# Performance work log

Measured on AMD Instinct MI355X. Metric: run time of the kernel, lower is better.

The kernel has to match this reference:

```python
import jax, jax.numpy as jnp
import numpy as np

D = 1024
H = 16
HD = D // H
FF = 4096
B = 4
S = 1024
EPS = 1e-5


def layer_norm(x, g, b):
    mu = jnp.mean(x, axis=-1, keepdims=True)
    var = jnp.mean(jnp.square(x - mu), axis=-1, keepdims=True)
    return (x - mu) * jax.lax.rsqrt(var + EPS) * g + b


def setup_inputs() -> dict:
    key = jax.random.key(0)
    ks = jax.random.split(key, 16)
    s = 0.02
    return {
        "src": jax.random.normal(ks[0], (B, S, D), jnp.float32),
        "attn_bias": jax.random.normal(ks[1], (H, S, S), jnp.float32),
        "Wqkv": jax.random.normal(ks[2], (3 * D, D), jnp.float32) * s,
        "bqkv": jnp.zeros((3 * D,), jnp.float32),
        "Wo": jax.random.normal(ks[3], (D, D), jnp.float32) * s,
        "bo": jnp.zeros((D,), jnp.float32),
        "g1": jnp.ones((D,), jnp.float32),
        "b1n": jnp.zeros((D,), jnp.float32),
        "g2": jnp.ones((D,), jnp.float32),
        "b2n": jnp.zeros((D,), jnp.float32),
        "W1": jax.random.normal(ks[4], (FF, D), jnp.float32) * s,
        "b1": jnp.zeros((FF,), jnp.float32),
        "W2": jax.random.normal(ks[5], (D, FF), jnp.float32) * s,
        "b2": jnp.zeros((D,), jnp.float32),
    }


def reference(src, attn_bias, Wqkv, bqkv, Wo, bo, g1, b1n, g2, b2n, W1, b1, W2, b2):
    bsz, seq, _ = src.shape
    qkv = src @ Wqkv.T + bqkv                      # [B,S,3D]
    q, k, v = jnp.split(qkv, 3, axis=-1)
    q = q.reshape(bsz, seq, H, HD)
    k = k.reshape(bsz, seq, H, HD)
    v = v.reshape(bsz, seq, H, HD)
    scores = jnp.einsum('bthd,bshd->bhts', q, k) / np.sqrt(HD).astype(np.float32)
    scores = scores + attn_bias[None]              # 3D bias broadcast over batch
    w = jax.nn.softmax(scores, axis=-1)
    ctx = jnp.einsum('bhts,bshd->bthd', w, v).reshape(bsz, seq, D)
    attn_out = ctx @ Wo.T + bo
    x = layer_norm(src + attn_out, g1, b1n)
    ff = (jax.nn.gelu(x @ W1.T + b1, approximate=False)) @ W2.T + b2
    return layer_norm(x + ff, g2, b2n)
```

## Files before the change

kernel.cpp:

```cpp
#include <hip/hip_runtime.h>
#include <cstdint>

typedef unsigned short u16;
typedef __bf16 bf16x8 __attribute__((ext_vector_type(8)));
typedef float f32x4 __attribute__((ext_vector_type(4)));
typedef unsigned short u16x8 __attribute__((ext_vector_type(8)));
typedef unsigned short u16x4 __attribute__((ext_vector_type(4)));

__device__ __forceinline__ u16 f2b(float f) {
  union { float f; unsigned u; } x; x.f = f;
  unsigned r = (x.u + 0x7FFFu + ((x.u >> 16) & 1u)) >> 16;
  return (u16)r;
}
__device__ __forceinline__ float b2f(u16 v) {
  union { unsigned u; float f; } x; x.u = (unsigned)v << 16; return x.f;
}

__device__ __forceinline__ void gload_lds16(const void* g, void* l) {
  __builtin_amdgcn_global_load_lds(
      (__attribute__((address_space(1))) void*)(uintptr_t)g,
      (__attribute__((address_space(3))) void*)(uintptr_t)l, 16, 0, 0);
}

struct CastArgs {
  const float* in[5];
  u16* out[5];
  int cum[6];
};
__global__ void cast_multi(CastArgs a) {
  const int i = blockIdx.x * 256 + threadIdx.x;
  int r = 0;
#pragma unroll
  for (int k = 1; k < 5; ++k) r += (i >= a.cum[k]);
  const int local = i - a.cum[r];
  const float4 v = *(const float4*)(a.in[r] + (size_t)local * 4);
  u16x4 o = {f2b(v.x), f2b(v.y), f2b(v.z), f2b(v.w)};
  *(u16x4*)(a.out[r] + (size_t)local * 4) = o;
}

template<bool GELU_ACT>
__global__ void gemm_nt(const u16* __restrict__ A, const u16* __restrict__ Bw,
                        const float* __restrict__ bias, u16* __restrict__ Cb,
                        int M, int N, int K) {
  __shared__ u16 As[2][128 * 32];
  __shared__ u16 Bs[2][128 * 32];
  const int tid = threadIdx.x;
  const int lane = tid & 63, wid = tid >> 6;
  const int bm = blockIdx.y * 128, bn = blockIdx.x * 128;
  const int wm = wid >> 1, wn = wid & 1;
  const int r = lane & 15, g = lane >> 4;
  const int s4 = (r >> 1) & 3;

  auto stage = [&](int buf, int k0) {
#pragma unroll
    for (int i = 0; i < 2; ++i) {
      const int c = tid + i * 256;
      const int row = c >> 2, ch = c & 3;
      const int gs = ch ^ ((row >> 1) & 3);
      gload_lds16(A + (size_t)(bm + row) * K + k0 + gs * 8, &As[buf][c * 8]);
      gload_lds16(Bw + (size_t)(bn + row) * K + k0 + gs * 8, &Bs[buf][c * 8]);
    }
  };

  f32x4 acc[4][4] = {};
  stage(0, 0);
  __syncthreads();
  const int nk = K >> 5;
  int cur = 0;
  for (int kt = 0; kt < nk; ++kt) {
    if (kt + 1 < nk) stage(cur ^ 1, (kt + 1) * 32);
    bf16x8 af[4], bfr[4];
#pragma unroll
    for (int m = 0; m < 4; ++m)
      af[m] = *(const bf16x8*)&As[cur][(wm * 64 + m * 16 + r) * 32 + (g ^ s4) * 8];
#pragma unroll
    for (int n = 0; n < 4; ++n)
      bfr[n] = *(const bf16x8*)&Bs[cur][(wn * 64 + n * 16 + r) * 32 + (g ^ s4) * 8];
#pragma unroll
    for (int m = 0; m < 4; ++m)
#pragma unroll
      for (int n = 0; n < 4; ++n)
        acc[m][n] = __builtin_amdgcn_mfma_f32_16x16x32_bf16(af[m], bfr[n], acc[m][n], 0, 0, 0);
    __syncthreads();
    cur ^= 1;
  }
#pragma unroll
  for (int m = 0; m < 4; ++m) {
    const int row0 = bm + wm * 64 + m * 16 + g * 4;
#pragma unroll
    for (int n = 0; n < 4; ++n) {
      const int col = bn + wn * 64 + n * 16 + r;
      const float bv = bias[col];
#pragma unroll
      for (int j = 0; j < 4; ++j) {
        float v = acc[m][n][j] + bv;
        if (GELU_ACT) v = 0.5f * v * (1.f + erff(v * 0.70710678118654752f));
        Cb[(size_t)(row0 + j) * N + col] = f2b(v);
      }
    }
  }
}

__global__ void gemm_nt_splitk(const u16* __restrict__ A, const u16* __restrict__ Bw,
                               float* __restrict__ parts, int M, int N, int K, int Kc) {
  __shared__ u16 As[2][128 * 32];
  __shared__ u16 Bs[2][128 * 32];
  const int tid = threadIdx.x;
  const int lane = tid & 63, wid = tid >> 6;
  const int bm = blockIdx.y * 128, bn = blockIdx.x * 128;
  const int kbase = blockIdx.z * Kc;
  const int wm = wid >> 1, wn = wid & 1;
  const int r = lane & 15, g = lane >> 4;
  const int s4 = (r >> 1) & 3;

  auto stage = [&](int buf, int k0) {
#pragma unroll
    for (int i = 0; i < 2; ++i) {
      const int c = tid + i * 256;
      const int row = c >> 2, ch = c & 3;
      const int gs = ch ^ ((row >> 1) & 3);
      gload_lds16(A + (size_t)(bm + row) * K + k0 + gs * 8, &As[buf][c * 8]);
      gload_lds16(Bw + (size_t)(bn + row) * K + k0 + gs * 8, &Bs[buf][c * 8]);
    }
  };

  f32x4 acc[4][4] = {};
  stage(0, kbase);
  __syncthreads();
  const int nk = Kc >> 5;
  int cur = 0;
  for (int kt = 0; kt < nk; ++kt) {
    if (kt + 1 < nk) stage(cur ^ 1, kbase + (kt + 1) * 32);
    bf16x8 af[4], bfr[4];
#pragma unroll
    for (int m = 0; m < 4; ++m)
      af[m] = *(const bf16x8*)&As[cur][(wm * 64 + m * 16 + r) * 32 + (g ^ s4) * 8];
#pragma unroll
    for (int n = 0; n < 4; ++n)
      bfr[n] = *(const bf16x8*)&Bs[cur][(wn * 64 + n * 16 + r) * 32 + (g ^ s4) * 8];
#pragma unroll
    for (int m = 0; m < 4; ++m)
#pragma unroll
      for (int n = 0; n < 4; ++n)
        acc[m][n] = __builtin_amdgcn_mfma_f32_16x16x32_bf16(af[m], bfr[n], acc[m][n], 0, 0, 0);
    __syncthreads();
    cur ^= 1;
  }
  float* Cp = parts + (size_t)blockIdx.z * M * N;
#pragma unroll
  for (int m = 0; m < 4; ++m) {
    const int row0 = bm + wm * 64 + m * 16 + g * 4;
#pragma unroll
    for (int n = 0; n < 4; ++n) {
      const int col = bn + wn * 64 + n * 16 + r;
#pragma unroll
      for (int j = 0; j < 4; ++j)
        Cp[(size_t)(row0 + j) * N + col] = acc[m][n][j];
    }
  }
}

__global__ void vtrans_kernel(const u16* __restrict__ qkv, u16* __restrict__ Vt) {
  const int bh = blockIdx.y, b = bh >> 4, h = bh & 15;
  const int s0 = blockIdx.x * 128;
  const int tid = threadIdx.x;
  __shared__ u16 t[128][66];
#pragma unroll
  for (int i = 0; i < 32; ++i) {
    const int e = tid + i * 256;
    const int s = e >> 6, d = e & 63;
    t[s][d] = qkv[(size_t)(b * 1024 + s0 + s) * 3072 + 2048 + h * 64 + d];
  }
  __syncthreads();
#pragma unroll
  for (int i = 0; i < 4; ++i) {
    const int c = tid + i * 256;
    const int d = c >> 4, scol = (c & 15) * 8;
    u16x8 v;
#pragma unroll
    for (int j = 0; j < 8; ++j) v[j] = t[scol + j][d];
    *(u16x8*)(Vt + ((size_t)bh * 64 + d) * 1024 + s0 + scol) = v;
  }
}

__global__ __launch_bounds__(256) void attn_kernel(
    const u16* __restrict__ qkv, const u16* __restrict__ Vt,
    const float* __restrict__ bias, u16* __restrict__ ctx) {
  const int yy = blockIdx.y;
  const int h = yy >> 2, b = yy & 3;
  const int q0 = blockIdx.x * 32;
  const int tid = threadIdx.x;
  const int lane = tid & 63, wid = tid >> 6;
  const int r = lane & 15, g = lane >> 4;
  const int bh = b * 16 + h;

  __shared__ __align__(16) u16 PB[2][16 * 1024];

  const size_t qb0 = (size_t)(b * 1024 + q0 + r) * 3072 + h * 64;
  const size_t qb1 = (size_t)(b * 1024 + q0 + 16 + r) * 3072 + h * 64;
  const bf16x8 aq00 = *(const bf16x8*)(qkv + qb0 + g * 8);
  const bf16x8 aq01 = *(const bf16x8*)(qkv + qb0 + 32 + g * 8);
  const bf16x8 aq10 = *(const bf16x8*)(qkv + qb1 + g * 8);
  const bf16x8 aq11 = *(const bf16x8*)(qkv + qb1 + 32 + g * 8);

  const int n0 = wid * 256;

#pragma unroll 4
  for (int nt = 0; nt < 16; ++nt) {
    const int key = n0 + nt * 16 + r;
    const size_t kbase = (size_t)(b * 1024 + key) * 3072 + 1024 + h * 64;
    const bf16x8 bk0 = *(const bf16x8*)(qkv + kbase + g * 8);
    const bf16x8 bk1 = *(const bf16x8*)(qkv + kbase + 32 + g * 8);
    f32x4 a0 = {0.f, 0.f, 0.f, 0.f}, a1 = {0.f, 0.f, 0.f, 0.f};
    a0 = __builtin_amdgcn_mfma_f32_16x16x32_bf16(bk0, aq00, a0, 0, 0, 0);
    a1 = __builtin_amdgcn_mfma_f32_16x16x32_bf16(bk0, aq10, a1, 0, 0, 0);
    a0 = __builtin_amdgcn_mfma_f32_16x16x32_bf16(bk1, aq01, a0, 0, 0, 0);
    a1 = __builtin_amdgcn_mfma_f32_16x16x32_bf16(bk1, aq11, a1, 0, 0, 0);
    const int col = n0 + nt * 16 + g * 4;
    const int idx = r * 1024 + (col ^ ((r & 15) << 3));
    u16x4 o0 = {f2b(a0[0] * 0.125f), f2b(a0[1] * 0.125f),
                f2b(a0[2] * 0.125f), f2b(a0[3] * 0.125f)};
    u16x4 o1 = {f2b(a1[0] * 0.125f), f2b(a1[1] * 0.125f),
                f2b(a1[2] * 0.125f), f2b(a1[3] * 0.125f)};
    *(u16x4*)&PB[0][idx] = o0;
    *(u16x4*)&PB[1][idx] = o1;
  }
  __syncthreads();

#pragma unroll
  for (int tr = 0; tr < 8; ++tr) {
    const int t = tr & 1, rr = tr >> 1;
    const int row = wid * 4 + rr;
    const int swz = (row & 15) << 3;
    u16* prow = &PB[t][row * 1024];
    const float* brow = bias + ((size_t)h * 1024 + q0 + t * 16 + row) * 1024;
    const int c0 = lane * 16;
    float bb[16];
    *(float4*)&bb[0]  = *(const float4*)(brow + c0);
    *(float4*)&bb[4]  = *(const float4*)(brow + c0 + 4);
    *(float4*)&bb[8]  = *(const float4*)(brow + c0 + 8);
    *(float4*)&bb[12] = *(const float4*)(brow + c0 + 12);
    const u16x8 v0 = *(const u16x8*)&prow[c0 ^ swz];
    const u16x8 v1 = *(const u16x8*)&prow[(c0 + 8) ^ swz];
    float f[16];
#pragma unroll
    for (int k = 0; k < 8; ++k) {
      f[k]     = b2f(v0[k]) + bb[k];
      f[8 + k] = b2f(v1[k]) + bb[8 + k];
    }
    float m = f[0];
#pragma unroll
    for (int k = 1; k < 16; ++k) m = fmaxf(m, f[k]);
    m = fmaxf(m, __shfl_xor(m, 1));  m = fmaxf(m, __shfl_xor(m, 2));
    m = fmaxf(m, __shfl_xor(m, 4));  m = fmaxf(m, __shfl_xor(m, 8));
    m = fmaxf(m, __shfl_xor(m, 16)); m = fmaxf(m, __shfl_xor(m, 32));
    float s = 0.f;
#pragma unroll
    for (int k = 0; k < 16; ++k) { f[k] = __expf(f[k] - m); s += f[k]; }
    s += __shfl_xor(s, 1);  s += __shfl_xor(s, 2);
    s += __shfl_xor(s, 4);  s += __shfl_xor(s, 8);
    s += __shfl_xor(s, 16); s += __shfl_xor(s, 32);
    const float inv = 1.f / s;
    u16x8 o0, o1;
#pragma unroll
    for (int k = 0; k < 8; ++k) {
      o0[k] = f2b(f[k] * inv);
      o1[k] = f2b(f[8 + k] * inv);
    }
    *(u16x8*)&prow[c0 ^ swz] = o0;
    *(u16x8*)&prow[(c0 + 8) ^ swz] = o1;
  }
  __syncthreads();

  f32x4 oa = {0.f, 0.f, 0.f, 0.f}, ob = {0.f, 0.f, 0.f, 0.f};
  const u16* vrow = Vt + ((size_t)bh * 64 + wid * 16 + r) * 1024;
#pragma unroll 4
  for (int ks = 0; ks < 32; ++ks) {
    const int off = (ks * 32 + g * 8) ^ ((r & 15) << 3);
    const bf16x8 vb = *(const bf16x8*)(vrow + ks * 32 + g * 8);
    const bf16x8 pa0 = *(const bf16x8*)&PB[0][r * 1024 + off];
    const bf16x8 pa1 = *(const bf16x8*)&PB[1][r * 1024 + off];
    oa = __builtin_amdgcn_mfma_f32_16x16x32_bf16(pa0, vb, oa, 0, 0, 0);
    ob = __builtin_amdgcn_mfma_f32_16x16x32_bf16(pa1, vb, ob, 0, 0, 0);
  }
#pragma unroll
  for (int j = 0; j < 4; ++j) {
    ctx[(size_t)(b * 1024 + q0 + g * 4 + j) * 1024 + h * 64 + wid * 16 + r] = f2b(oa[j]);
    ctx[(size_t)(b * 1024 + q0 + 16 + g * 4 + j) * 1024 + h * 64 + wid * 16 + r] = f2b(ob[j]);
  }
}

template<int NP>
__global__ void ln_sum_kernel(const float* __restrict__ parts,
                              const float* __restrict__ resid,
                              const float* __restrict__ cbias,
                              const float* __restrict__ gw, const float* __restrict__ bw,
                              float* __restrict__ outf, u16* __restrict__ outb) {
  const int row = blockIdx.x, tid = threadIdx.x;
  const size_t off = (size_t)row * 1024 + tid * 4;
  float4 v = *(const float4*)(resid + off);
  const float4 cb = *(const float4*)(cbias + tid * 4);
  v.x += cb.x; v.y += cb.y; v.z += cb.z; v.w += cb.w;
#pragma unroll
  for (int p = 0; p < NP; ++p) {
    const float4 a = *(const float4*)(parts + (size_t)p * 4096 * 1024 + off);
    v.x += a.x; v.y += a.y; v.z += a.z; v.w += a.w;
  }
  float s = v.x + v.y + v.z + v.w;
  float q = v.x * v.x + v.y * v.y + v.z * v.z + v.w * v.w;
#pragma unroll
  for (int m = 32; m >= 1; m >>= 1) { s += __shfl_xor(s, m); q += __shfl_xor(q, m); }
  __shared__ float rs[4], rq[4];
  if ((tid & 63) == 0) { rs[tid >> 6] = s; rq[tid >> 6] = q; }
  __syncthreads();
  s = rs[0] + rs[1] + rs[2] + rs[3];
  q = rq[0] + rq[1] + rq[2] + rq[3];
  const float mu = s * (1.f / 1024.f);
  const float inv = rsqrtf(q * (1.f / 1024.f) - mu * mu + 1e-5f);
  const float4 g4 = *(const float4*)(gw + tid * 4);
  const float4 b4 = *(const float4*)(bw + tid * 4);
  float4 o;
  o.x = (v.x - mu) * inv * g4.x + b4.x;
  o.y = (v.y - mu) * inv * g4.y + b4.y;
  o.z = (v.z - mu) * inv * g4.z + b4.z;
  o.w = (v.w - mu) * inv * g4.w + b4.w;
  if (outf) *(float4*)(outf + off) = o;
  if (outb) {
    u16x4 ob = {f2b(o.x), f2b(o.y), f2b(o.z), f2b(o.w)};
    *(u16x4*)(outb + off) = ob;
  }
}

extern "C" void kernel_launch(void* const* d_in, const int* in_sizes, int n_in,
                              void* d_out, int out_size, void* d_ws, size_t ws_size,
                              hipStream_t stream) {
  (void)in_sizes; (void)n_in; (void)out_size; (void)ws_size;
  const float* src   = (const float*)d_in[0];
  const float* abias = (const float*)d_in[1];
  const float* Wqkv  = (const float*)d_in[2];
  const float* bqkv  = (const float*)d_in[3];
  const float* Wo    = (const float*)d_in[4];
  const float* bo    = (const float*)d_in[5];
  const float* g1    = (const float*)d_in[6];
  const float* b1n   = (const float*)d_in[7];
  const float* g2    = (const float*)d_in[8];
  const float* b2n   = (const float*)d_in[9];
  const float* W1    = (const float*)d_in[10];
  const float* b1    = (const float*)d_in[11];
  const float* W2    = (const float*)d_in[12];
  const float* b2    = (const float*)d_in[13];
  float* out = (float*)d_out;

  char* ws = (char*)d_ws;
  const size_t MB = 1024 * 1024;
  u16* srcb  = (u16*)(ws + 0 * MB);
  u16* ctxb  = (u16*)(ws + 0 * MB);
  u16* xb    = (u16*)(ws + 0 * MB);
  u16* Wqkvb = (u16*)(ws + 8 * MB);
  u16* Wob   = (u16*)(ws + 14 * MB);
  float* xf  = (float*)(ws + 8 * MB);
  u16* W2b   = (u16*)(ws + 24 * MB);
  u16* qkvb  = (u16*)(ws + 32 * MB);
  u16* Vt    = (u16*)(ws + 56 * MB);
  u16* hb    = (u16*)(ws + 32 * MB);
  float* parts = (float*)(ws + 64 * MB);
  u16* W1b   = (u16*)(ws + 96 * MB);

  CastArgs ca;
  ca.in[0] = src;  ca.out[0] = srcb;
  ca.in[1] = Wqkv; ca.out[1] = Wqkvb;
  ca.in[2] = Wo;   ca.out[2] = Wob;
  ca.in[3] = W1;   ca.out[3] = W1b;
  ca.in[4] = W2;   ca.out[4] = W2b;
  ca.cum[0] = 0;
  ca.cum[1] = 1048576;
  ca.cum[2] = 1048576 + 786432;
  ca.cum[3] = 1048576 + 786432 + 262144;
  ca.cum[4] = 1048576 + 786432 + 262144 + 1048576;
  ca.cum[5] = 4194304;
  cast_multi<<<4194304 / 256, 256, 0, stream>>>(ca);

  gemm_nt<false><<<dim3(3072 / 128, 4096 / 128), 256, 0, stream>>>(
      srcb, Wqkvb, bqkv, qkvb, 4096, 3072, 1024);
  vtrans_kernel<<<dim3(8, 64), 256, 0, stream>>>(qkvb, Vt);
  attn_kernel<<<dim3(32, 64), 256, 0, stream>>>(qkvb, Vt, abias, ctxb);
  gemm_nt_splitk<<<dim3(1024 / 128, 4096 / 128, 2), 256, 0, stream>>>(
      ctxb, Wob, parts, 4096, 1024, 1024, 512);
  ln_sum_kernel<2><<<4096, 256, 0, stream>>>(parts, src, bo, g1, b1n, xf, xb);
  gemm_nt<true><<<dim3(4096 / 128, 4096 / 128), 256, 0, stream>>>(
      xb, W1b, b1, hb, 4096, 4096, 1024);
  gemm_nt_splitk<<<dim3(1024 / 128, 4096 / 128, 2), 256, 0, stream>>>(
      hb, W2b, parts, 4096, 1024, 4096, 2048);
  ln_sum_kernel<2><<<4096, 256, 0, stream>>>(parts, xf, b2, g2, b2n, out, nullptr);
}
```

Before: 295.5 us.

## Double attention block to 512 threads and split work across eight waves

Raises the attention kernel from 4 to 8 waves per block. Each wave now handles half as many key tiles in QK^T, four softmax rows instead of eight, and one 16-row query tile against a 16-column d slice in PV. The PV loop splits its k-steps across two accumulators that are summed before the store. This aims to hide more latency within a block, but 64KB of LDS per block already caps residency, so the gain depends on per-block parallelism and risks extra register pressure at 512 threads.

```diff
diff --git a/kernel.cpp b/kernel.cpp
--- a/kernel.cpp
+++ b/kernel.cpp
@@ -183,7 +183,7 @@
   }
 }
 
-__global__ __launch_bounds__(256) void attn_kernel(
+__global__ __launch_bounds__(512) void attn_kernel(
     const u16* __restrict__ qkv, const u16* __restrict__ Vt,
     const float* __restrict__ bias, u16* __restrict__ ctx) {
   const int yy = blockIdx.y;
@@ -203,10 +203,10 @@
   const bf16x8 aq10 = *(const bf16x8*)(qkv + qb1 + g * 8);
   const bf16x8 aq11 = *(const bf16x8*)(qkv + qb1 + 32 + g * 8);
 
-  const int n0 = wid * 256;
+  const int n0 = wid * 128;
 
 #pragma unroll 4
-  for (int nt = 0; nt < 16; ++nt) {
+  for (int nt = 0; nt < 8; ++nt) {
     const int key = n0 + nt * 16 + r;
     const size_t kbase = (size_t)(b * 1024 + key) * 3072 + 1024 + h * 64;
     const bf16x8 bk0 = *(const bf16x8*)(qkv + kbase + g * 8);
@@ -228,12 +228,12 @@
   __syncthreads();
 
 #pragma unroll
-  for (int tr = 0; tr < 8; ++tr) {
-    const int t = tr & 1, rr = tr >> 1;
-    const int row = wid * 4 + rr;
-    const int swz = (row & 15) << 3;
-    u16* prow = &PB[t][row * 1024];
-    const float* brow = bias + ((size_t)h * 1024 + q0 + t * 16 + row) * 1024;
+  for (int rr = 0; rr < 4; ++rr) {
+    const int gr = wid * 4 + rr;
+    const int t = gr >> 4, lr = gr & 15;
+    const int swz = lr << 3;
+    u16* prow = &PB[t][lr * 1024];
+    const float* brow = bias + ((size_t)h * 1024 + q0 + gr) * 1024;
     const int c0 = lane * 16;
     float bb[16];
     *(float4*)&bb[0]  = *(const float4*)(brow + c0);
@@ -272,22 +272,25 @@
   }
   __syncthreads();
 
+  const int t = wid >> 2, dt = wid & 3;
   f32x4 oa = {0.f, 0.f, 0.f, 0.f}, ob = {0.f, 0.f, 0.f, 0.f};
-  const u16* vrow = Vt + ((size_t)bh * 64 + wid * 16 + r) * 1024;
+  const u16* vrow = Vt + ((size_t)bh * 64 + dt * 16 + r) * 1024;
+  const u16* prow = &PB[t][r * 1024];
 #pragma unroll 4
-  for (int ks = 0; ks < 32; ++ks) {
-    const int off = (ks * 32 + g * 8) ^ ((r & 15) << 3);
-    const bf16x8 vb = *(const bf16x8*)(vrow + ks * 32 + g * 8);
-    const bf16x8 pa0 = *(const bf16x8*)&PB[0][r * 1024 + off];
-    const bf16x8 pa1 = *(const bf16x8*)&PB[1][r * 1024 + off];
-    oa = __builtin_amdgcn_mfma_f32_16x16x32_bf16(pa0, vb, oa, 0, 0, 0);
-    ob = __builtin_amdgcn_mfma_f32_16x16x32_bf16(pa1, vb, ob, 0, 0, 0);
-  }
-#pragma unroll
-  for (int j = 0; j < 4; ++j) {
-    ctx[(size_t)(b * 1024 + q0 + g * 4 + j) * 1024 + h * 64 + wid * 16 + r] = f2b(oa[j]);
-    ctx[(size_t)(b * 1024 + q0 + 16 + g * 4 + j) * 1024 + h * 64 + wid * 16 + r] = f2b(ob[j]);
-  }
+  for (int ks = 0; ks < 32; ks += 2) {
+    const int off0 = (ks * 32 + g * 8) ^ ((r & 15) << 3);
+    const int off1 = ((ks + 1) * 32 + g * 8) ^ ((r & 15) << 3);
+    const bf16x8 pa0 = *(const bf16x8*)&prow[off0];
+    const bf16x8 vb0 = *(const bf16x8*)(vrow + ks * 32 + g * 8);
+    oa = __builtin_amdgcn_mfma_f32_16x16x32_bf16(pa0, vb0, oa, 0, 0, 0);
+    const bf16x8 pa1 = *(const bf16x8*)&prow[off1];
+    const bf16x8 vb1 = *(const bf16x8*)(vrow + (ks + 1) * 32 + g * 8);
+    ob = __builtin_amdgcn_mfma_f32_16x16x32_bf16(pa1, vb1, ob, 0, 0, 0);
+  }
+#pragma unroll
+  for (int j = 0; j < 4; ++j)
+    ctx[(size_t)(b * 1024 + q0 + t * 16 + g * 4 + j) * 1024 + h * 64 + dt * 16 + r] =
+        f2b(oa[j] + ob[j]);
 }
 
 template<int NP>
@@ -383,7 +386,7 @@
   gemm_nt<false><<<dim3(3072 / 128, 4096 / 128), 256, 0, stream>>>(
       srcb, Wqkvb, bqkv, qkvb, 4096, 3072, 1024);
   vtrans_kernel<<<dim3(8, 64), 256, 0, stream>>>(qkvb, Vt);
-  attn_kernel<<<dim3(32, 64), 256, 0, stream>>>(qkvb, Vt, abias, ctxb);
+  attn_kernel<<<dim3(32, 64), 512, 0, stream>>>(qkvb, Vt, abias, ctxb);
   gemm_nt_splitk<<<dim3(1024 / 128, 4096 / 128, 2), 256, 0, stream>>>(
       ctxb, Wob, parts, 4096, 1024, 1024, 512);
   ln_sum_kernel<2><<<4096, 256, 0, stream>>>(parts, src, bo, g1, b1n, xf, xb);
```

Result: slower. 320.3 us (+8.4%).

## Fuse V transpose into QKV GEMM epilogue and bias add into score stage

Applied to the files above, without the earlier changes.

The QKV GEMM epilogue now writes the V columns directly in transposed [b,h,d,s] layout, so the separate vtrans kernel launch and its extra read/write of V are gone. In attention, the bias is loaded per MFMA tile and added before the bf16 rounding of the scores, instead of being re-read in the softmax pass. Risks: the V stores in the GEMM are 4-element strided writes, which are less coalesced. The bias is also now folded in before rounding to bf16, which slightly changes numerics.

```diff
diff --git a/kernel.cpp b/kernel.cpp
--- a/kernel.cpp
+++ b/kernel.cpp
@@ -38,10 +38,10 @@
   *(u16x4*)(a.out[r] + (size_t)local * 4) = o;
 }
 
-template<bool GELU_ACT>
+template<bool GELU_ACT, bool WRITE_VT>
 __global__ void gemm_nt(const u16* __restrict__ A, const u16* __restrict__ Bw,
                         const float* __restrict__ bias, u16* __restrict__ Cb,
-                        int M, int N, int K) {
+                        u16* __restrict__ Vt, int M, int N, int K) {
   __shared__ u16 As[2][128 * 32];
   __shared__ u16 Bs[2][128 * 32];
   const int tid = threadIdx.x;
@@ -91,11 +91,20 @@
     for (int n = 0; n < 4; ++n) {
       const int col = bn + wn * 64 + n * 16 + r;
       const float bv = bias[col];
-#pragma unroll
-      for (int j = 0; j < 4; ++j) {
-        float v = acc[m][n][j] + bv;
-        if (GELU_ACT) v = 0.5f * v * (1.f + erff(v * 0.70710678118654752f));
-        Cb[(size_t)(row0 + j) * N + col] = f2b(v);
+      if (WRITE_VT && col >= 2048) {
+        const int hv = col - 2048;
+        const int bb = row0 >> 10, s0 = row0 & 1023;
+        u16x4 ov;
+#pragma unroll
+        for (int j = 0; j < 4; ++j) ov[j] = f2b(acc[m][n][j] + bv);
+        *(u16x4*)(Vt + (((size_t)(bb * 16 + (hv >> 6))) * 64 + (hv & 63)) * 1024 + s0) = ov;
+      } else {
+#pragma unroll
+        for (int j = 0; j < 4; ++j) {
+          float v = acc[m][n][j] + bv;
+          if (GELU_ACT) v = 0.5f * v * (1.f + erff(v * 0.70710678118654752f));
+          Cb[(size_t)(row0 + j) * N + col] = f2b(v);
+        }
       }
     }
   }
@@ -160,29 +169,6 @@
   }
 }
 
-__global__ void vtrans_kernel(const u16* __restrict__ qkv, u16* __restrict__ Vt) {
-  const int bh = blockIdx.y, b = bh >> 4, h = bh & 15;
-  const int s0 = blockIdx.x * 128;
-  const int tid = threadIdx.x;
-  __shared__ u16 t[128][66];
-#pragma unroll
-  for (int i = 0; i < 32; ++i) {
-    const int e = tid + i * 256;
-    const int s = e >> 6, d = e & 63;
-    t[s][d] = qkv[(size_t)(b * 1024 + s0 + s) * 3072 + 2048 + h * 64 + d];
-  }
-  __syncthreads();
-#pragma unroll
-  for (int i = 0; i < 4; ++i) {
-    const int c = tid + i * 256;
-    const int d = c >> 4, scol = (c & 15) * 8;
-    u16x8 v;
-#pragma unroll
-    for (int j = 0; j < 8; ++j) v[j] = t[scol + j][d];
-    *(u16x8*)(Vt + ((size_t)bh * 64 + d) * 1024 + s0 + scol) = v;
-  }
-}
-
 __global__ __launch_bounds__(256) void attn_kernel(
     const u16* __restrict__ qkv, const u16* __restrict__ Vt,
     const float* __restrict__ bias, u16* __restrict__ ctx) {
@@ -204,6 +190,8 @@
   const bf16x8 aq11 = *(const bf16x8*)(qkv + qb1 + 32 + g * 8);
 
   const int n0 = wid * 256;
+  const float* brow0 = bias + ((size_t)h * 1024 + q0 + r) * 1024;
+  const float* brow1 = brow0 + 16 * 1024;
 
 #pragma unroll 4
   for (int nt = 0; nt < 16; ++nt) {
@@ -211,17 +199,19 @@
     const size_t kbase = (size_t)(b * 1024 + key) * 3072 + 1024 + h * 64;
     const bf16x8 bk0 = *(const bf16x8*)(qkv + kbase + g * 8);
     const bf16x8 bk1 = *(const bf16x8*)(qkv + kbase + 32 + g * 8);
+    const int col = n0 + nt * 16 + g * 4;
+    const float4 bb0 = *(const float4*)(brow0 + col);
+    const float4 bb1 = *(const float4*)(brow1 + col);
     f32x4 a0 = {0.f, 0.f, 0.f, 0.f}, a1 = {0.f, 0.f, 0.f, 0.f};
     a0 = __builtin_amdgcn_mfma_f32_16x16x32_bf16(bk0, aq00, a0, 0, 0, 0);
     a1 = __builtin_amdgcn_mfma_f32_16x16x32_bf16(bk0, aq10, a1, 0, 0, 0);
     a0 = __builtin_amdgcn_mfma_f32_16x16x32_bf16(bk1, aq01, a0, 0, 0, 0);
     a1 = __builtin_amdgcn_mfma_f32_16x16x32_bf16(bk1, aq11, a1, 0, 0, 0);
-    const int col = n0 + nt * 16 + g * 4;
     const int idx = r * 1024 + (col ^ ((r & 15) << 3));
-    u16x4 o0 = {f2b(a0[0] * 0.125f), f2b(a0[1] * 0.125f),
-                f2b(a0[2] * 0.125f), f2b(a0[3] * 0.125f)};
-    u16x4 o1 = {f2b(a1[0] * 0.125f), f2b(a1[1] * 0.125f),
-                f2b(a1[2] * 0.125f), f2b(a1[3] * 0.125f)};
+    u16x4 o0 = {f2b(fmaf(a0[0], 0.125f, bb0.x)), f2b(fmaf(a0[1], 0.125f, bb0.y)),
+                f2b(fmaf(a0[2], 0.125f, bb0.z)), f2b(fmaf(a0[3], 0.125f, bb0.w))};
+    u16x4 o1 = {f2b(fmaf(a1[0], 0.125f, bb1.x)), f2b(fmaf(a1[1], 0.125f, bb1.y)),
+                f2b(fmaf(a1[2], 0.125f, bb1.z)), f2b(fmaf(a1[3], 0.125f, bb1.w))};
     *(u16x4*)&PB[0][idx] = o0;
     *(u16x4*)&PB[1][idx] = o1;
   }
@@ -233,21 +223,12 @@
     const int row = wid * 4 + rr;
     const int swz = (row & 15) << 3;
     u16* prow = &PB[t][row * 1024];
-    const float* brow = bias + ((size_t)h * 1024 + q0 + t * 16 + row) * 1024;
     const int c0 = lane * 16;
-    float bb[16];
-    *(float4*)&bb[0]  = *(const float4*)(brow + c0);
-    *(float4*)&bb[4]  = *(const float4*)(brow + c0 + 4);
-    *(float4*)&bb[8]  = *(const float4*)(brow + c0 + 8);
-    *(float4*)&bb[12] = *(const float4*)(brow + c0 + 12);
     const u16x8 v0 = *(const u16x8*)&prow[c0 ^ swz];
     const u16x8 v1 = *(const u16x8*)&prow[(c0 + 8) ^ swz];
     float f[16];
 #pragma unroll
-    for (int k = 0; k < 8; ++k) {
-      f[k]     = b2f(v0[k]) + bb[k];
-      f[8 + k] = b2f(v1[k]) + bb[8 + k];
-    }
+    for (int k = 0; k < 8; ++k) { f[k] = b2f(v0[k]); f[8 + k] = b2f(v1[k]); }
     float m = f[0];
 #pragma unroll
     for (int k = 1; k < 16; ++k) m = fmaxf(m, f[k]);
@@ -380,15 +361,14 @@
   ca.cum[5] = 4194304;
   cast_multi<<<4194304 / 256, 256, 0, stream>>>(ca);
 
-  gemm_nt<false><<<dim3(3072 / 128, 4096 / 128), 256, 0, stream>>>(
-      srcb, Wqkvb, bqkv, qkvb, 4096, 3072, 1024);
-  vtrans_kernel<<<dim3(8, 64), 256, 0, stream>>>(qkvb, Vt);
+  gemm_nt<false, true><<<dim3(3072 / 128, 4096 / 128), 256, 0, stream>>>(
+      srcb, Wqkvb, bqkv, qkvb, Vt, 4096, 3072, 1024);
   attn_kernel<<<dim3(32, 64), 256, 0, stream>>>(qkvb, Vt, abias, ctxb);
   gemm_nt_splitk<<<dim3(1024 / 128, 4096 / 128, 2), 256, 0, stream>>>(
       ctxb, Wob, parts, 4096, 1024, 1024, 512);
   ln_sum_kernel<2><<<4096, 256, 0, stream>>>(parts, src, bo, g1, b1n, xf, xb);
-  gemm_nt<true><<<dim3(4096 / 128, 4096 / 128), 256, 0, stream>>>(
-      xb, W1b, b1, hb, 4096, 4096, 1024);
+  gemm_nt<true, false><<<dim3(4096 / 128, 4096 / 128), 256, 0, stream>>>(
+      xb, W1b, b1, hb, nullptr, 4096, 4096, 1024);
   gemm_nt_splitk<<<dim3(1024 / 128, 4096 / 128, 2), 256, 0, stream>>>(
       hb, W2b, parts, 4096, 1024, 4096, 2048);
   ln_sum_kernel<2><<<4096, 256, 0, stream>>>(parts, xf, b2, g2, b2n, out, nullptr);
```

Result: no change. 296.6 us (+0.4%).
